# Kernel tuning notes

Hardware: AMD Instinct MI355X
Metric: run time of the kernel (lower is better)

The kernel has to match this reference:

```python
import jax, jax.numpy as jnp
import numpy as np

B, T = 4096, 2048

def setup_inputs() -> dict:
    key = jax.random.key(0)
    k1, k2, k3 = jax.random.split(key, 3)
    pred = jax.random.normal(k1, (B, T), dtype=jnp.float32)  # predicted log-durations
    # alignment = ground-truth durations (strictly positive, log is taken)
    alignment = jax.random.uniform(k2, (B, T), dtype=jnp.float32, minval=1.0, maxval=20.0)
    token_lengths = jax.random.randint(k3, (B,), 1, T + 1)  # valid lengths in [1, T]
    return {"pred": pred, "alignment": alignment, "token_lengths": token_lengths}

def reference(pred, alignment, token_lengths):
    # Masked per-sample MSE over the first token_lengths[i] positions,
    # then mean over the batch (matches the python loop exactly).
    Tdim = pred.shape[1]
    mask = jnp.arange(Tdim)[None, :] < token_lengths[:, None]          # [B, T] bool
    diff = jnp.where(mask, pred - jnp.log(alignment), 0.0)             # padded alignment > 0, log is safe
    per_sample_mse = jnp.sum(diff * diff, axis=1) / token_lengths.astype(pred.dtype)  # [B]
    return jnp.mean(per_sample_mse)
```

## Files before the change

kernel.cpp:

```cpp
#include <hip/hip_runtime.h>


__global__ __launch_bounds__(512) void dploss_fused_kernel(
    const float* __restrict__ pred,
    const float* __restrict__ align,
    const int* __restrict__ lens,
    float* __restrict__ out,
    int B, int T)
{
    const int gtid = blockIdx.x * blockDim.x + threadIdx.x;
    const int wave = gtid >> 6;
    const int lane = threadIdx.x & 63;
    const int wave_in_block = threadIdx.x >> 6;

    float row_mse = 0.0f;

    if (wave < B) {
        const int row = wave;
        const int L = lens[row];
        const float4* __restrict__ p4 = (const float4*)(pred + (size_t)row * T);
        const float4* __restrict__ a4 = (const float4*)(align + (size_t)row * T);
        const int ngroups = (L + 3) >> 2;

        float acc = 0.0f;
        for (int g = lane; g < ngroups; g += 64) {
            float4 p = p4[g];
            float4 a = a4[g];
            const int base = g << 2;
            if (base + 4 <= L) {
                float d0 = p.x - __logf(a.x);
                float d1 = p.y - __logf(a.y);
                float d2 = p.z - __logf(a.z);
                float d3 = p.w - __logf(a.w);
                acc += d0 * d0 + d1 * d1 + d2 * d2 + d3 * d3;
            } else {
                if (base + 0 < L) { float d = p.x - __logf(a.x); acc += d * d; }
                if (base + 1 < L) { float d = p.y - __logf(a.y); acc += d * d; }
                if (base + 2 < L) { float d = p.z - __logf(a.z); acc += d * d; }
            }
        }

        #pragma unroll
        for (int off = 32; off > 0; off >>= 1)
            acc += __shfl_down(acc, off, 64);

        row_mse = acc / (float)L;
    }

    __shared__ float wsum[8];
    if (lane == 0) wsum[wave_in_block] = row_mse;
    __syncthreads();

    if (threadIdx.x == 0) {
        float total = 0.0f;
        #pragma unroll
        for (int w = 0; w < 8; ++w) total += wsum[w];
        atomicAdd(out, total / (float)B);
    }
}

extern "C" void kernel_launch(void* const* d_in, const int* in_sizes, int n_in,
                              void* d_out, int out_size, void* d_ws, size_t ws_size,
                              hipStream_t stream)
{
    const float* pred  = (const float*)d_in[0];
    const float* align = (const float*)d_in[1];
    const int*   lens  = (const int*)d_in[2];

    const int B = in_sizes[2];
    const int T = in_sizes[0] / B;

    float* out = (float*)d_out;

    hipMemsetAsync(out, 0, sizeof(float), stream);

    const int threads = 512;
    const int waves_per_block = threads / 64;
    const int grid = (B + waves_per_block - 1) / waves_per_block;

    dploss_fused_kernel<<<grid, threads, 0, stream>>>(pred, align, lens, out, B, T);
}
```

Before: 96.64 us.

## Flatten 16 variable-length rows per block into one load-balanced work list

Instead of assigning one wave per row, each 1024-thread block takes 16 rows, builds a prefix sum of their float4 group counts in shared memory, and spreads the concatenated groups evenly across all threads. Each element's contribution is scaled by its row's 1/L so one block-wide reduction is enough. This removes the load imbalance between waves caused by random row lengths, and removes the idle lanes on short rows. In exchange, every element now does a 15-step search through the prefix sums, and the kernel has extra shared-memory setup and syncs.

```diff
diff --git a/kernel.cpp b/kernel.cpp
--- a/kernel.cpp
+++ b/kernel.cpp
@@ -1,61 +1,88 @@
 #include <hip/hip_runtime.h>
 
 
-__global__ __launch_bounds__(512) void dploss_fused_kernel(
+#define ROWS_PER_BLOCK 16
+
+__global__ __launch_bounds__(1024) void dploss_fused_kernel(
     const float* __restrict__ pred,
     const float* __restrict__ align,
     const int* __restrict__ lens,
     float* __restrict__ out,
     int B, int T)
 {
-    const int gtid = blockIdx.x * blockDim.x + threadIdx.x;
-    const int wave = gtid >> 6;
-    const int lane = threadIdx.x & 63;
-    const int wave_in_block = threadIdx.x >> 6;
+    __shared__ int   l_len[ROWS_PER_BLOCK];
+    __shared__ float l_inv[ROWS_PER_BLOCK];
+    __shared__ int   l_pre[ROWS_PER_BLOCK + 1];
+    __shared__ float wsum[16];
 
-    float row_mse = 0.0f;
+    const int row0 = blockIdx.x * ROWS_PER_BLOCK;
+    const int tid  = threadIdx.x;
 
-    if (wave < B) {
-        const int row = wave;
-        const int L = lens[row];
-        const float4* __restrict__ p4 = (const float4*)(pred + (size_t)row * T);
-        const float4* __restrict__ a4 = (const float4*)(align + (size_t)row * T);
-        const int ngroups = (L + 3) >> 2;
+    if (tid < ROWS_PER_BLOCK) {
+        const int row = row0 + tid;
+        int L = (row < B) ? lens[row] : 0;
+        l_len[tid] = L;
+        l_inv[tid] = (L > 0) ? (1.0f / (float)L) : 0.0f;
+    }
+    __syncthreads();
+    if (tid == 0) {
+        int run = 0;
+        #pragma unroll
+        for (int r = 0; r < ROWS_PER_BLOCK; ++r) {
+            l_pre[r] = run;
+            run += (l_len[r] + 3) >> 2;
+        }
+        l_pre[ROWS_PER_BLOCK] = run;
+    }
+    __syncthreads();
 
-        float acc = 0.0f;
-        for (int g = lane; g < ngroups; g += 64) {
-            float4 p = p4[g];
-            float4 a = a4[g];
-            const int base = g << 2;
-            if (base + 4 <= L) {
-                float d0 = p.x - __logf(a.x);
-                float d1 = p.y - __logf(a.y);
-                float d2 = p.z - __logf(a.z);
-                float d3 = p.w - __logf(a.w);
-                acc += d0 * d0 + d1 * d1 + d2 * d2 + d3 * d3;
-            } else {
-                if (base + 0 < L) { float d = p.x - __logf(a.x); acc += d * d; }
-                if (base + 1 < L) { float d = p.y - __logf(a.y); acc += d * d; }
-                if (base + 2 < L) { float d = p.z - __logf(a.z); acc += d * d; }
-            }
+    const int total = l_pre[ROWS_PER_BLOCK];
+    float acc = 0.0f;
+
+    for (int gf = tid; gf < total; gf += 1024) {
+        int r = 0;
+        #pragma unroll
+        for (int k = 1; k < ROWS_PER_BLOCK; ++k)
+            r += (gf >= l_pre[k]) ? 1 : 0;
+
+        const int   g    = gf - l_pre[r];
+        const int   L    = l_len[r];
+        const float invL = l_inv[r];
+        const size_t off = (size_t)(row0 + r) * T;
+        const float4 p = ((const float4*)(pred  + off))[g];
+        const float4 a = ((const float4*)(align + off))[g];
+        const int base = g << 2;
+
+        float s;
+        if (base + 4 <= L) {
+            float d0 = p.x - __logf(a.x);
+            float d1 = p.y - __logf(a.y);
+            float d2 = p.z - __logf(a.z);
+            float d3 = p.w - __logf(a.w);
+            s = d0 * d0 + d1 * d1 + d2 * d2 + d3 * d3;
+        } else {
+            s = 0.0f;
+            if (base + 0 < L) { float d = p.x - __logf(a.x); s += d * d; }
+            if (base + 1 < L) { float d = p.y - __logf(a.y); s += d * d; }
+            if (base + 2 < L) { float d = p.z - __logf(a.z); s += d * d; }
         }
-
-        #pragma unroll
-        for (int off = 32; off > 0; off >>= 1)
-            acc += __shfl_down(acc, off, 64);
-
-        row_mse = acc / (float)L;
+        acc += s * invL;
     }
 
-    __shared__ float wsum[8];
-    if (lane == 0) wsum[wave_in_block] = row_mse;
+    #pragma unroll
+    for (int o = 32; o > 0; o >>= 1)
+        acc += __shfl_down(acc, o, 64);
+
+    const int lane = tid & 63;
+    const int wave = tid >> 6;
+    if (lane == 0) wsum[wave] = acc;
     __syncthreads();
 
-    if (threadIdx.x == 0) {
-        float total = 0.0f;
+    if (tid == 0) {
+        float t = 0.0f;
         #pragma unroll
-        for (int w = 0; w < 8; ++w) total += wsum[w];
-        atomicAdd(out, total / (float)B);
+        for (int w = 0; w < 16; ++w) t += wsum[w];
+        atomicAdd(out, t / (float)B);
     }
 }
 
@@ -74,9 +101,6 @@
 
     hipMemsetAsync(out, 0, sizeof(float), stream);
 
-    const int threads = 512;
-    const int waves_per_block = threads / 64;
-    const int grid = (B + waves_per_block - 1) / waves_per_block;
-
-    dploss_fused_kernel<<<grid, threads, 0, stream>>>(pred, align, lens, out, B, T);
+    const int grid = (B + ROWS_PER_BLOCK - 1) / ROWS_PER_BLOCK;
+    dploss_fused_kernel<<<grid, 1024, 0, stream>>>(pred, align, lens, out, B, T);
 }
```

Result: no change. 96.15 us (-0.5%).
